# Kernel optimization log

Hardware: AMD Instinct MI355X
Metric: run time of the kernel (lower is better)

Reference implementation:

```python
import jax, jax.numpy as jnp
import numpy as np

B, S, U = 64, 64, 16
EMB = 10
D = U - 2 + 2 * EMB      # encoder d_model = 34
DD = 3                   # decoder d_model
FF = 4                   # dim_feedforward
NL = 4                   # num layers (enc and dec)
ENH = 2                  # encoder heads
WV, SV = 10000, 400      # word / syllable vocab sizes


def _ln(x, w, b, eps=1e-5):
    mu = jnp.mean(x, -1, keepdims=True)
    var = jnp.mean((x - mu) ** 2, -1, keepdims=True)
    return (x - mu) / jnp.sqrt(var + eps) * w + b


def _mha(xq, xkv, qkv_w, qkv_b, out_w, out_b, nhead, mask=None):
    d = xq.shape[-1]
    wq, wk, wv = jnp.split(qkv_w, 3, axis=0)
    bq, bk, bv = jnp.split(qkv_b, 3, axis=0)
    q = xq @ wq.T + bq
    k = xkv @ wk.T + bk
    v = xkv @ wv.T + bv
    b_, sq, sk = q.shape[0], q.shape[1], k.shape[1]
    dh = d // nhead
    q = q.reshape(b_, sq, nhead, dh)
    k = k.reshape(b_, sk, nhead, dh)
    v = v.reshape(b_, sk, nhead, dh)
    scores = jnp.einsum('bqhd,bkhd->bhqk', q, k) * (1.0 / np.sqrt(dh))
    if mask is not None:
        scores = scores + mask
    attn = jax.nn.softmax(scores, axis=-1)
    out = jnp.einsum('bhqk,bkhd->bqhd', attn, v).reshape(b_, sq, d)
    return out @ out_w.T + out_b


def _pos_encoding(batch, d_model):
    # Faithful to the original quirk: pe has shape [max_len, 1, d] and is added
    # to a batch-first [B,S,D] tensor as x + pe[:B]  ->  row b of pe is added
    # to ALL sequence positions of batch element b.
    pos = jnp.arange(batch, dtype=jnp.float32)[:, None]
    div = jnp.exp(jnp.arange(0, d_model, 2, dtype=jnp.float32) * (-np.log(10000.0) / d_model))
    ang = pos * div  # [B, D/2]
    pe = jnp.stack([jnp.sin(ang), jnp.cos(ang)], axis=-1).reshape(batch, d_model)
    return pe[:, None, :]  # [B,1,D]


def setup_inputs() -> dict:
    key = jax.random.key(0)
    ks = iter(jax.random.split(key, 64))

    def n(shape, s=0.1):
        return jax.random.normal(next(ks), shape, dtype=jnp.float32) * s

    base = jax.random.uniform(next(ks), (B, S, U), dtype=jnp.float32)
    widx = jax.random.randint(next(ks), (B, S), 0, WV).astype(jnp.float32)
    sidx = jax.random.randint(next(ks), (B, S), 0, SV).astype(jnp.float32)
    src = base.at[:, :, U - 2].set(widx).at[:, :, U - 1].set(sidx)
    return {
        'src': src,
        'word_emb': jax.random.uniform(next(ks), (WV, EMB), jnp.float32, -0.1, 0.1),
        'syll_emb': jax.random.uniform(next(ks), (SV, EMB), jnp.float32, -0.1, 0.1),
        'enc_qkv_w': n((NL, 3 * D, D)), 'enc_qkv_b': jnp.zeros((NL, 3 * D)),
        'enc_out_w': n((NL, D, D)), 'enc_out_b': jnp.zeros((NL, D)),
        'enc_ln1_w': jnp.ones((NL, D)), 'enc_ln1_b': jnp.zeros((NL, D)),
        'enc_lin1_w': n((NL, FF, D)), 'enc_lin1_b': jnp.zeros((NL, FF)),
        'enc_lin2_w': n((NL, D, FF)), 'enc_lin2_b': jnp.zeros((NL, D)),
        'enc_ln2_w': jnp.ones((NL, D)), 'enc_ln2_b': jnp.zeros((NL, D)),
        'norm_w': jnp.ones((D,)), 'norm_b': jnp.zeros((D,)),
        'eo_w': jax.random.uniform(next(ks), (DD, D), jnp.float32, -0.1, 0.1),
        'eo_b': jnp.zeros((DD,)),
        'dec_sa_qkv_w': n((NL, 3 * DD, DD)), 'dec_sa_qkv_b': jnp.zeros((NL, 3 * DD)),
        'dec_sa_out_w': n((NL, DD, DD)), 'dec_sa_out_b': jnp.zeros((NL, DD)),
        'dec_ln1_w': jnp.ones((NL, DD)), 'dec_ln1_b': jnp.zeros((NL, DD)),
        'dec_ca_qkv_w': n((NL, 3 * DD, DD)), 'dec_ca_qkv_b': jnp.zeros((NL, 3 * DD)),
        'dec_ca_out_w': n((NL, DD, DD)), 'dec_ca_out_b': jnp.zeros((NL, DD)),
        'dec_ln2_w': jnp.ones((NL, DD)), 'dec_ln2_b': jnp.zeros((NL, DD)),
        'dec_lin1_w': n((NL, FF, DD)), 'dec_lin1_b': jnp.zeros((NL, FF)),
        'dec_lin2_w': n((NL, DD, FF)), 'dec_lin2_b': jnp.zeros((NL, DD)),
        'dec_ln3_w': jnp.ones((NL, DD)), 'dec_ln3_b': jnp.zeros((NL, DD)),
    }


def reference(src, word_emb, syll_emb,
              enc_qkv_w, enc_qkv_b, enc_out_w, enc_out_b,
              enc_ln1_w, enc_ln1_b, enc_lin1_w, enc_lin1_b,
              enc_lin2_w, enc_lin2_b, enc_ln2_w, enc_ln2_b,
              norm_w, norm_b, eo_w, eo_b,
              dec_sa_qkv_w, dec_sa_qkv_b, dec_sa_out_w, dec_sa_out_b,
              dec_ln1_w, dec_ln1_b,
              dec_ca_qkv_w, dec_ca_qkv_b, dec_ca_out_w, dec_ca_out_b,
              dec_ln2_w, dec_ln2_b,
              dec_lin1_w, dec_lin1_b, dec_lin2_w, dec_lin2_b,
              dec_ln3_w, dec_ln3_b):
    b, s = src.shape[0], src.shape[1]
    # embed_lyrics
    widx = src[:, :, U - 2].astype(jnp.int32)
    sidx = src[:, :, U - 1].astype(jnp.int32)
    x = jnp.concatenate([src[:, :, :U - 2], word_emb[widx], syll_emb[sidx]], axis=2)  # [B,S,D]
    x = x + _pos_encoding(b, D)
    # TransformerEncoder (post-norm, relu, dropout=0) + final LayerNorm
    for l in range(NL):
        sa = _mha(x, x, enc_qkv_w[l], enc_qkv_b[l], enc_out_w[l], enc_out_b[l], ENH)
        x = _ln(x + sa, enc_ln1_w[l], enc_ln1_b[l])
        ff = jax.nn.relu(x @ enc_lin1_w[l].T + enc_lin1_b[l]) @ enc_lin2_w[l].T + enc_lin2_b[l]
        x = _ln(x + ff, enc_ln2_w[l], enc_ln2_b[l])
    x = _ln(x, norm_w, norm_b)
    memory = x @ eo_w.T + eo_b  # [B,S,3]

    causal = jnp.where(jnp.tril(jnp.ones((s, s), bool)), 0.0, -1e9).astype(jnp.float32)

    def decode(tgt):
        y = tgt
        for l in range(NL):
            sa = _mha(y, y, dec_sa_qkv_w[l], dec_sa_qkv_b[l], dec_sa_out_w[l], dec_sa_out_b[l], 1, causal)
            y = _ln(y + sa, dec_ln1_w[l], dec_ln1_b[l])
            ca = _mha(y, memory, dec_ca_qkv_w[l], dec_ca_qkv_b[l], dec_ca_out_w[l], dec_ca_out_b[l], 1)
            y = _ln(y + ca, dec_ln2_w[l], dec_ln2_b[l])
            ff = jax.nn.relu(y @ dec_lin1_w[l].T + dec_lin1_b[l]) @ dec_lin2_w[l].T + dec_lin2_b[l]
            y = _ln(y + ff, dec_ln3_w[l], dec_ln3_b[l])
        return y

    # mask, position i only depends on tgt[:, :i+1], so a fixed-size padded
    # buffer + scan computes identical values.
    def step(tgt, i):
        out_i = jax.lax.dynamic_slice_in_dim(decode(tgt), i, 1, axis=1)  # [B,1,3]
        return jax.lax.dynamic_update_slice(tgt, out_i, (0, i + 1, 0)), None

    tgt0 = jnp.zeros((b, s, DD), jnp.float32)
    tgt, _ = jax.lax.scan(step, tgt0, jnp.arange(s - 1))
    return jnp.concatenate([tgt, src[:, :, U - 2:U - 1], src[:, :, U - 1:U]], axis=2)
```

## Files before the change

### kernel.cpp

```cpp
#include <hip/hip_runtime.h>
#include <math.h>

#define B_ 64
#define S_ 64
#define U_ 16
#define EMB_ 10
#define D_ 34
#define DD_ 3
#define FF_ 4
#define NL_ 4

typedef float v2f __attribute__((ext_vector_type(2)));

__global__ __launch_bounds__(512) void enc_kernel(
    const float* __restrict__ src, const float* __restrict__ wemb,
    const float* __restrict__ semb,
    const float* __restrict__ qkv_w, const float* __restrict__ qkv_b,
    const float* __restrict__ out_w, const float* __restrict__ out_b,
    const float* __restrict__ ln1_w, const float* __restrict__ ln1_b,
    const float* __restrict__ lin1_w, const float* __restrict__ lin1_b,
    const float* __restrict__ lin2_w, const float* __restrict__ lin2_b,
    const float* __restrict__ ln2_w, const float* __restrict__ ln2_b,
    const float* __restrict__ norm_w, const float* __restrict__ norm_b,
    const float* __restrict__ eo_w, const float* __restrict__ eo_b,
    float* __restrict__ mem, float* __restrict__ out)
{
    const int b = blockIdx.x;
    const int tid = threadIdx.x;
    const int wv_ = tid >> 6;
    const int lane = tid & 63;

    __shared__ float xs[S_][D_ + 1];
    __shared__ float tmp[S_][D_ + 1];
    __shared__ float att[S_][D_ + 1];
    __shared__ __align__(16) float qsh[2][S_][21];
    __shared__ __align__(16) float ksh[2][S_][20];
    __shared__ __align__(16) float vsh[2][S_][20];
    __shared__ float ffh[S_][5];
    __shared__ float pacc[4][128][19];

    const float rs17 = 0.24253562503633297f;
    const float negln = -logf(10000.0f) / (float)D_;

    #pragma unroll
    for (int rr = 0; rr < 5; ++rr) {
        int idx = tid + rr * 512;
        if (idx < S_ * D_) {
            int pos = idx / D_, d = idx % D_;
            float v;
            if (d < U_ - 2) {
                v = src[(b * S_ + pos) * U_ + d];
            } else if (d < U_ - 2 + EMB_) {
                int wi = (int)src[(b * S_ + pos) * U_ + (U_ - 2)];
                v = wemb[wi * EMB_ + (d - (U_ - 2))];
            } else {
                int si = (int)src[(b * S_ + pos) * U_ + (U_ - 1)];
                v = semb[si * EMB_ + (d - (U_ - 2 + EMB_))];
            }
            int k = d >> 1;
            float div = __expf((float)(2 * k) * negln);
            float ang = (float)b * div;
            v += (d & 1) ? __cosf(ang) : __sinf(ang);
            xs[pos][d] = v;
        }
    }
    __syncthreads();

    for (int l = 0; l < NL_; ++l) {
        const float* Wq = qkv_w + l * 3 * D_ * D_;
        const float* Bq = qkv_b + l * 3 * D_;

        {
            v2f xr2[17];
            #pragma unroll
            for (int d2 = 0; d2 < 17; ++d2) {
                v2f t; t.x = xs[lane][2 * d2]; t.y = xs[lane][2 * d2 + 1];
                xr2[d2] = t;
            }
            #pragma unroll
            for (int rb = 0; rb < 13; ++rb) {
                int r = wv_ + (rb << 3);
                if (r < 3 * D_) {
                    int ru = __builtin_amdgcn_readfirstlane(r);
                    const v2f* w2 = (const v2f*)(Wq + ru * D_);
                    v2f a2; a2.x = Bq[ru]; a2.y = 0.f;
                    #pragma unroll
                    for (int d2 = 0; d2 < 17; ++d2)
                        a2 = __builtin_elementwise_fma(xr2[d2], w2[d2], a2);
                    float acc = a2.x + a2.y;
                    if (ru < D_)          { int h = (ru >= 17), dd = ru - h * 17; qsh[h][lane][dd] = acc; }
                    else if (ru < 2 * D_) { int rr2 = ru - D_;     int h = (rr2 >= 17), dd = rr2 - h * 17; ksh[h][lane][dd] = acc; }
                    else                  { int rr2 = ru - 2 * D_; int h = (rr2 >= 17), dd = rr2 - h * 17; vsh[h][lane][dd] = acc; }
                }
            }
        }
        __syncthreads();

        {
            int c = tid >> 7, hq = tid & 127;
            int h = hq >> 6, qi = hq & 63;
            float qv[17], acc[17];
            #pragma unroll
            for (int d = 0; d < 17; ++d) { qv[d] = qsh[h][qi][d]; acc[d] = 0.f; }
            float ssum = 0.f;
            int j0 = c * 16;
            #pragma unroll 4
            for (int jj = 0; jj < 16; ++jj) {
                int j = j0 + jj;
                const float4* kr = (const float4*)ksh[h][j];
                const float4* vr = (const float4*)vsh[h][j];
                float4 k0 = kr[0], k1 = kr[1], k2 = kr[2], k3 = kr[3];
                float  k16 = ksh[h][j][16];
                float4 v0 = vr[0], v1 = vr[1], v2 = vr[2], v3 = vr[3];
                float  v16 = vsh[h][j][16];
                float sE = qv[0]*k0.x + qv[2]*k0.z + qv[4]*k1.x + qv[6]*k1.z +
                           qv[8]*k2.x + qv[10]*k2.z + qv[12]*k3.x + qv[14]*k3.z;
                float sO = qv[1]*k0.y + qv[3]*k0.w + qv[5]*k1.y + qv[7]*k1.w +
                           qv[9]*k2.y + qv[11]*k2.w + qv[13]*k3.y + qv[15]*k3.w;
                float sc = sE + sO + qv[16]*k16;
                float e = __expf(sc * rs17);
                ssum += e;
                acc[0] += e*v0.x;  acc[1] += e*v0.y;  acc[2] += e*v0.z;  acc[3] += e*v0.w;
                acc[4] += e*v1.x;  acc[5] += e*v1.y;  acc[6] += e*v1.z;  acc[7] += e*v1.w;
                acc[8] += e*v2.x;  acc[9] += e*v2.y;  acc[10] += e*v2.z; acc[11] += e*v2.w;
                acc[12] += e*v3.x; acc[13] += e*v3.y; acc[14] += e*v3.z; acc[15] += e*v3.w;
                acc[16] += e*v16;
            }
            #pragma unroll
            for (int d = 0; d < 17; ++d) pacc[c][hq][d] = acc[d];
            pacc[c][hq][17] = ssum;
        }
        __syncthreads();

        if (tid < 128) {
            int h = tid >> 6, qi = tid & 63;
            int off = h * 17;
            float ssum = pacc[0][tid][17] + pacc[1][tid][17] +
                         pacc[2][tid][17] + pacc[3][tid][17];
            float inv = 1.f / ssum;
            #pragma unroll
            for (int d = 0; d < 17; ++d)
                att[qi][off + d] = (pacc[0][tid][d] + pacc[1][tid][d] +
                                    pacc[2][tid][d] + pacc[3][tid][d]) * inv;
        }
        __syncthreads();

        {
            v2f ar2[17];
            #pragma unroll
            for (int d2 = 0; d2 < 17; ++d2) {
                v2f t; t.x = att[lane][2 * d2]; t.y = att[lane][2 * d2 + 1];
                ar2[d2] = t;
            }
            const float* Wo = out_w + l * D_ * D_;
            const float* Bo = out_b + l * D_;
            #pragma unroll
            for (int rb = 0; rb < 5; ++rb) {
                int d = wv_ + (rb << 3);
                if (d < D_) {
                    int du = __builtin_amdgcn_readfirstlane(d);
                    const v2f* w2 = (const v2f*)(Wo + du * D_);
                    v2f a2; a2.x = Bo[du]; a2.y = 0.f;
                    #pragma unroll
                    for (int d2 = 0; d2 < 17; ++d2)
                        a2 = __builtin_elementwise_fma(ar2[d2], w2[d2], a2);
                    tmp[lane][du] = xs[lane][du] + a2.x + a2.y;
                }
            }
        }
        __syncthreads();

        {
            int row = tid >> 3, sub = tid & 7;
            float s = 0.f, sq = 0.f;
            #pragma unroll
            for (int d = sub; d < D_; d += 8) { float t = tmp[row][d]; s += t; sq = fmaf(t, t, sq); }
            #pragma unroll
            for (int m = 1; m < 8; m <<= 1) { s += __shfl_xor(s, m, 8); sq += __shfl_xor(sq, m, 8); }
            float mu = s * (1.0f / D_);
            float var = fmaf(sq, 1.0f / D_, -mu * mu);
            float rstd = rsqrtf(var + 1e-5f);
            #pragma unroll
            for (int d = sub; d < D_; d += 8)
                xs[row][d] = (tmp[row][d] - mu) * rstd * ln1_w[l * D_ + d] + ln1_b[l * D_ + d];
        }
        __syncthreads();

        if (wv_ < 4) {
            int fu = __builtin_amdgcn_readfirstlane(wv_);
            const v2f* w2 = (const v2f*)(lin1_w + l * FF_ * D_ + fu * D_);
            v2f a2; a2.x = lin1_b[l * FF_ + fu]; a2.y = 0.f;
            #pragma unroll
            for (int d2 = 0; d2 < 17; ++d2) {
                v2f t; t.x = xs[lane][2 * d2]; t.y = xs[lane][2 * d2 + 1];
                a2 = __builtin_elementwise_fma(t, w2[d2], a2);
            }
            ffh[lane][fu] = fmaxf(a2.x + a2.y, 0.f);
        }
        __syncthreads();

        {
            float h0 = ffh[lane][0], h1 = ffh[lane][1],
                  h2 = ffh[lane][2], h3 = ffh[lane][3];
            const float* W2 = lin2_w + l * D_ * FF_;
            const float* B2 = lin2_b + l * D_;
            #pragma unroll
            for (int rb = 0; rb < 5; ++rb) {
                int d = wv_ + (rb << 3);
                if (d < D_) {
                    int du = __builtin_amdgcn_readfirstlane(d);
                    const float* wrow = W2 + du * FF_;
                    float acc = fmaf(h0, wrow[0], fmaf(h1, wrow[1],
                                fmaf(h2, wrow[2], fmaf(h3, wrow[3], B2[du]))));
                    tmp[lane][du] = xs[lane][du] + acc;
                }
            }
        }
        __syncthreads();

        {
            int row = tid >> 3, sub = tid & 7;
            float s = 0.f, sq = 0.f;
            #pragma unroll
            for (int d = sub; d < D_; d += 8) { float t = tmp[row][d]; s += t; sq = fmaf(t, t, sq); }
            #pragma unroll
            for (int m = 1; m < 8; m <<= 1) { s += __shfl_xor(s, m, 8); sq += __shfl_xor(sq, m, 8); }
            float mu = s * (1.0f / D_);
            float var = fmaf(sq, 1.0f / D_, -mu * mu);
            float rstd = rsqrtf(var + 1e-5f);
            #pragma unroll
            for (int d = sub; d < D_; d += 8)
                xs[row][d] = (tmp[row][d] - mu) * rstd * ln2_w[l * D_ + d] + ln2_b[l * D_ + d];
        }
        __syncthreads();
    }

    {
        int row = tid >> 3, sub = tid & 7;
        float s = 0.f, sq = 0.f;
        #pragma unroll
        for (int d = sub; d < D_; d += 8) { float t = xs[row][d]; s += t; sq = fmaf(t, t, sq); }
        #pragma unroll
        for (int m = 1; m < 8; m <<= 1) { s += __shfl_xor(s, m, 8); sq += __shfl_xor(sq, m, 8); }
        float mu = s * (1.0f / D_);
        float var = fmaf(sq, 1.0f / D_, -mu * mu);
        float rstd = rsqrtf(var + 1e-5f);
        #pragma unroll
        for (int d = sub; d < D_; d += 8)
            tmp[row][d] = (xs[row][d] - mu) * rstd * norm_w[d] + norm_b[d];
    }
    __syncthreads();

    if (wv_ < 3) {
        int ru = __builtin_amdgcn_readfirstlane(wv_);
        const v2f* w2 = (const v2f*)(eo_w + ru * D_);
        v2f a2; a2.x = eo_b[ru]; a2.y = 0.f;
        #pragma unroll
        for (int d2 = 0; d2 < 17; ++d2) {
            v2f t; t.x = tmp[lane][2 * d2]; t.y = tmp[lane][2 * d2 + 1];
            a2 = __builtin_elementwise_fma(t, w2[d2], a2);
        }
        mem[(b * S_ + lane) * DD_ + ru] = a2.x + a2.y;
    }

    if (tid < S_) {
        out[(b * S_ + tid) * 5 + 3] = src[(b * S_ + tid) * U_ + (U_ - 2)];
        out[(b * S_ + tid) * 5 + 4] = src[(b * S_ + tid) * U_ + (U_ - 1)];
    }
}

#define PIN(x) asm volatile("" : "+v"(x))

template <int N> struct IC { static constexpr int value = N; };

template <int CTRL>
__device__ __forceinline__ void dpp4(float& a, float& b, float& c, float& d) {
    int ta = __builtin_amdgcn_update_dpp(0, __float_as_int(a), CTRL, 0xf, 0xf, true);
    int tb = __builtin_amdgcn_update_dpp(0, __float_as_int(b), CTRL, 0xf, 0xf, true);
    int tc = __builtin_amdgcn_update_dpp(0, __float_as_int(c), CTRL, 0xf, 0xf, true);
    int td = __builtin_amdgcn_update_dpp(0, __float_as_int(d), CTRL, 0xf, 0xf, true);
    a += __int_as_float(ta);
    b += __int_as_float(tb);
    c += __int_as_float(tc);
    d += __int_as_float(td);
}

__device__ __forceinline__ void red16_4(float& a, float& b, float& c, float& d) {
    dpp4<0x111>(a, b, c, d);
    dpp4<0x112>(a, b, c, d);
    dpp4<0x114>(a, b, c, d);
    dpp4<0x118>(a, b, c, d);
}

template <int L>
__device__ __forceinline__ float rlane(float v) {
    return __int_as_float(__builtin_amdgcn_readlane(__float_as_int(v), L));
}

__device__ __forceinline__ void ln3e(float z0, float z1, float z2,
                                     float w0, float w1, float w2,
                                     float b0, float b1, float b2,
                                     float& o0, float& o1, float& o2) {
    float s1 = (z0 + z1) + z2;
    float s2 = fmaf(z0, z0, fmaf(z1, z1, z2 * z2));
    float mu = s1 * (1.0f / 3.0f);
    float vpe = fmaf(s2, (1.0f / 3.0f), fmaf(-mu, mu, 1e-5f));
    float rstd = __builtin_amdgcn_rsqf(vpe);
    o0 = fmaf(z0 - mu, rstd * w0, b0);
    o1 = fmaf(z1 - mu, rstd * w1, b1);
    o2 = fmaf(z2 - mu, rstd * w2, b2);
}

__global__ __launch_bounds__(64, 1) void dec_kernel(
    const float* __restrict__ mem,
    const float* __restrict__ sa_qkv_w, const float* __restrict__ sa_qkv_b,
    const float* __restrict__ sa_out_w, const float* __restrict__ sa_out_b,
    const float* __restrict__ gln1_w, const float* __restrict__ gln1_b,
    const float* __restrict__ ca_qkv_w, const float* __restrict__ ca_qkv_b,
    const float* __restrict__ ca_out_w, const float* __restrict__ ca_out_b,
    const float* __restrict__ gln2_w, const float* __restrict__ gln2_b,
    const float* __restrict__ l1_w, const float* __restrict__ l1_b,
    const float* __restrict__ l2_w, const float* __restrict__ l2_b,
    const float* __restrict__ gln3_w, const float* __restrict__ gln3_b,
    float* __restrict__ out)
{
    const int b = blockIdx.x;
    const int lane = threadIdx.x;
    const float LOG2E = 1.4426950408889634f;
    const float rs3 = 0.5773502691896258f;
    const float QS = rs3 * LOG2E;

    float Wsq[NL_][6][3], Bsq[NL_][6];
    float Wvp[NL_][3][3], Bvp[NL_][3];
    float Bso[NL_][3];
    float N1w[NL_][3], N1bF[NL_][3];
    float N2w[NL_][3], N2bF[NL_][3];
    float wcu[NL_][3];
    float swcu[NL_];
    float cbb[NL_];
    float cvp[NL_][3];
    float W1N[NL_][4][3], b1n[NL_][4];
    float W2r[NL_][3][4];
    float N3w[NL_][3], N3b[NL_][3];

    #pragma unroll
    for (int l = 0; l < NL_; ++l) {
        #pragma unroll
        for (int r = 0; r < 6; ++r) {
            float sc = (r < 3) ? QS : 1.0f;
            Bsq[l][r] = sa_qkv_b[l * 9 + r] * sc;
            #pragma unroll
            for (int c = 0; c < 3; ++c) Wsq[l][r][c] = sa_qkv_w[l * 27 + r * 3 + c] * sc;
        }
        #pragma unroll
        for (int r = 0; r < 3; ++r) {
            float w0 = sa_out_w[l * 9 + r * 3 + 0];
            float w1 = sa_out_w[l * 9 + r * 3 + 1];
            float w2 = sa_out_w[l * 9 + r * 3 + 2];
            Bvp[l][r] = w0 * sa_qkv_b[l * 9 + 6] + w1 * sa_qkv_b[l * 9 + 7] + w2 * sa_qkv_b[l * 9 + 8];
            #pragma unroll
            for (int c = 0; c < 3; ++c)
                Wvp[l][r][c] = w0 * sa_qkv_w[l * 27 + 6 * 3 + c] +
                               w1 * sa_qkv_w[l * 27 + 7 * 3 + c] +
                               w2 * sa_qkv_w[l * 27 + 8 * 3 + c];
        }
        #pragma unroll
        for (int r = 0; r < 3; ++r) {
            Bso[l][r]  = sa_out_b[l * 3 + r];
            N1w[l][r]  = gln1_w[l * 3 + r];
            N1bF[l][r] = gln1_b[l * 3 + r] + ca_out_b[l * 3 + r];
            N2w[l][r]  = gln2_w[l * 3 + r];
            N2bF[l][r] = gln2_b[l * 3 + r] + l2_b[l * 3 + r];
            N3w[l][r]  = gln3_w[l * 3 + r];
            N3b[l][r]  = gln3_b[l * 3 + r];
        }
        #pragma unroll
        for (int j = 0; j < 4; ++j) {
            #pragma unroll
            for (int c = 0; c < 3; ++c)
                W1N[l][j][c] = l1_w[l * 12 + j * 3 + c] * gln2_w[l * 3 + c];
            b1n[l][j] = l1_w[l * 12 + j * 3 + 0] * gln2_b[l * 3 + 0] +
                        l1_w[l * 12 + j * 3 + 1] * gln2_b[l * 3 + 1] +
                        l1_w[l * 12 + j * 3 + 2] * gln2_b[l * 3 + 2] + l1_b[l * 4 + j];
        }
        #pragma unroll
        for (int r = 0; r < 3; ++r)
            #pragma unroll
            for (int j = 0; j < 4; ++j)
                W2r[l][r][j] = l2_w[l * 12 + r * 4 + j];
    }

    float m0 = mem[(b * S_ + lane) * DD_ + 0];
    float m1 = mem[(b * S_ + lane) * DD_ + 1];
    float m2 = mem[(b * S_ + lane) * DD_ + 2];

    #pragma unroll
    for (int l = 0; l < NL_; ++l) {
        float ck[3], cv[3], cuv[3];
        #pragma unroll
        for (int r = 0; r < 3; ++r) {
            ck[r] = ca_qkv_w[l * 27 + (3 + r) * 3 + 0] * m0 +
                    ca_qkv_w[l * 27 + (3 + r) * 3 + 1] * m1 +
                    ca_qkv_w[l * 27 + (3 + r) * 3 + 2] * m2 + ca_qkv_b[l * 9 + 3 + r];
            cv[r] = ca_qkv_w[l * 27 + (6 + r) * 3 + 0] * m0 +
                    ca_qkv_w[l * 27 + (6 + r) * 3 + 1] * m1 +
                    ca_qkv_w[l * 27 + (6 + r) * 3 + 2] * m2 + ca_qkv_b[l * 9 + 6 + r];
        }
        #pragma unroll
        for (int s = 0; s < 3; ++s)
            cuv[s] = QS * (ca_qkv_w[l * 27 + 0 + s] * ck[0] +
                           ca_qkv_w[l * 27 + 3 + s] * ck[1] +
                           ca_qkv_w[l * 27 + 6 + s] * ck[2]);
        float cbv = QS * (ca_qkv_b[l * 9 + 0] * ck[0] +
                          ca_qkv_b[l * 9 + 1] * ck[1] +
                          ca_qkv_b[l * 9 + 2] * ck[2]);
        #pragma unroll
        for (int r = 0; r < 3; ++r)
            cvp[l][r] = ca_out_w[l * 9 + r * 3 + 0] * cv[0] +
                        ca_out_w[l * 9 + r * 3 + 1] * cv[1] +
                        ca_out_w[l * 9 + r * 3 + 2] * cv[2];
        #pragma unroll
        for (int r = 0; r < 3; ++r) wcu[l][r] = cuv[r] * N1w[l][r];
        swcu[l] = wcu[l][0] + wcu[l][1] + wcu[l][2];
        cbb[l]  = cbv + cuv[0] * gln1_b[l * 3 + 0] + cuv[1] * gln1_b[l * 3 + 1]
                      + cuv[2] * gln1_b[l * 3 + 2];
    }

    #pragma unroll
    for (int l = 0; l < NL_; ++l) {
        #pragma unroll
        for (int r = 0; r < 6; ++r) {
            PIN(Bsq[l][r]);
            #pragma unroll
            for (int c = 0; c < 3; ++c) PIN(Wsq[l][r][c]);
        }
        PIN(swcu[l]); PIN(cbb[l]);
        #pragma unroll
        for (int r = 0; r < 3; ++r) {
            PIN(Bvp[l][r]); PIN(Bso[l][r]);
            PIN(N1w[l][r]); PIN(N1bF[l][r]); PIN(N2w[l][r]); PIN(N2bF[l][r]);
            PIN(N3w[l][r]); PIN(N3b[l][r]);
            PIN(wcu[l][r]); PIN(cvp[l][r]);
            #pragma unroll
            for (int c = 0; c < 3; ++c) PIN(Wvp[l][r][c]);
            #pragma unroll
            for (int j = 0; j < 4; ++j) PIN(W2r[l][r][j]);
        }
        #pragma unroll
        for (int j = 0; j < 4; ++j) {
            PIN(b1n[l][j]);
            #pragma unroll
            for (int c = 0; c < 3; ++c) PIN(W1N[l][j][c]);
        }
    }

    float sk[NL_][3] = {{0.f}}, sv[NL_][3] = {{0.f}};

    if (lane < 3) out[(b * S_ + 0) * 5 + lane] = 0.f;

    float y0 = 0.f, y1 = 0.f, y2 = 0.f;

    auto run_range = [&](int ibeg, int iend, auto nstc) {
        constexpr int NST = decltype(nstc)::value;
        constexpr int RL = (NST == 4) ? 15 : (NST == 5) ? 31 : 63;
        for (int i = ibeg; i < iend; ++i) {
            float msa = (lane <= i) ? 0.f : -1.0e30f;
            bool isme = (lane == i);
            #pragma unroll
            for (int l = 0; l < NL_; ++l) {
                float q[3], kn[3], vp[3];
                #pragma unroll
                for (int r = 0; r < 3; ++r) {
                    kn[r] = fmaf(Wsq[l][3 + r][0], y0, fmaf(Wsq[l][3 + r][1], y1, fmaf(Wsq[l][3 + r][2], y2, Bsq[l][3 + r])));
                    q[r]  = fmaf(Wsq[l][r][0], y0, fmaf(Wsq[l][r][1], y1, fmaf(Wsq[l][r][2], y2, Bsq[l][r])));
                    vp[r] = fmaf(Wvp[l][r][0], y0, fmaf(Wvp[l][r][1], y1, fmaf(Wvp[l][r][2], y2, Bvp[l][r])));
                }
                if (isme) {
                    #pragma unroll
                    for (int r = 0; r < 3; ++r) { sk[l][r] = kn[r]; sv[l][r] = vp[r]; }
                }
                float sc = fmaf(q[0], sk[l][0], fmaf(q[1], sk[l][1], fmaf(q[2], sk[l][2], msa)));
                float e = __builtin_amdgcn_exp2f(sc);
                float se = e;
                float sa0 = e * sv[l][0];
                float sa1 = e * sv[l][1];
                float sa2 = e * sv[l][2];
                red16_4(se, sa0, sa1, sa2);
                if constexpr (NST >= 5) dpp4<0x142>(se, sa0, sa1, sa2);
                if constexpr (NST >= 6) dpp4<0x143>(se, sa0, sa1, sa2);
                float es = rlane<RL>(se);
                float S0 = rlane<RL>(sa0), S1 = rlane<RL>(sa1), S2 = rlane<RL>(sa2);
                float yb0 = y0 + Bso[l][0], yb1 = y1 + Bso[l][1], yb2 = y2 + Bso[l][2];
                float z0 = fmaf(yb0, es, S0), z1 = fmaf(yb1, es, S1), z2v = fmaf(yb2, es, S2);
                float ee = es * es;

                float s1m = (z0 + z1) + z2v;
                float mu = s1m * (1.0f / 3.0f);
                float zw = fmaf(z0, wcu[l][0], fmaf(z1, wcu[l][1], z2v * wcu[l][2]));
                float inner = fmaf(-mu, swcu[l], zw);
                float s2m = fmaf(z0, z0, fmaf(z1, z1, z2v * z2v));
                float vpe = fmaf(s2m, (1.0f / 3.0f), fmaf(-mu, mu, 1e-5f * ee));
                float rstd1 = __builtin_amdgcn_rsqf(vpe);
                float sc2 = fmaf(rstd1, inner, cbb[l]);
                float e2 = __builtin_amdgcn_exp2f(sc2);
                float ce = e2;
                float ca0 = e2 * cvp[l][0];
                float ca1 = e2 * cvp[l][1];
                float ca2 = e2 * cvp[l][2];
                red16_4(ce, ca0, ca1, ca2);
                dpp4<0x142>(ce, ca0, ca1, ca2);
                dpp4<0x143>(ce, ca0, ca1, ca2);
                float yc0 = fmaf(z0 - mu, rstd1 * N1w[l][0], N1bF[l][0]);
                float yc1 = fmaf(z1 - mu, rstd1 * N1w[l][1], N1bF[l][1]);
                float yc2 = fmaf(z2v - mu, rstd1 * N1w[l][2], N1bF[l][2]);
                float cs = rlane<63>(ce);
                float C0 = rlane<63>(ca0), C1 = rlane<63>(ca1), C2 = rlane<63>(ca2);
                float g0 = fmaf(yc0, cs, C0), g1 = fmaf(yc1, cs, C1), g2 = fmaf(yc2, cs, C2);
                float cee = cs * cs;

                float t1m = (g0 + g1) + g2;
                float mu2 = t1m * (1.0f / 3.0f);
                float c20 = g0 - mu2, c21 = g1 - mu2, c22 = g2 - mu2;
                float t2m = fmaf(g0, g0, fmaf(g1, g1, g2 * g2));
                float vpe2 = fmaf(t2m, (1.0f / 3.0f), fmaf(-mu2, mu2, 1e-5f * cee));
                float rstd2 = __builtin_amdgcn_rsqf(vpe2);
                float d0 = fmaf(W1N[l][0][0], c20, fmaf(W1N[l][0][1], c21, W1N[l][0][2] * c22));
                float d1 = fmaf(W1N[l][1][0], c20, fmaf(W1N[l][1][1], c21, W1N[l][1][2] * c22));
                float d2 = fmaf(W1N[l][2][0], c20, fmaf(W1N[l][2][1], c21, W1N[l][2][2] * c22));
                float d3 = fmaf(W1N[l][3][0], c20, fmaf(W1N[l][3][1], c21, W1N[l][3][2] * c22));
                float h0 = fmaxf(fmaf(rstd2, d0, b1n[l][0]), 0.f);
                float h1 = fmaxf(fmaf(rstd2, d1, b1n[l][1]), 0.f);
                float h2 = fmaxf(fmaf(rstd2, d2, b1n[l][2]), 0.f);
                float h3 = fmaxf(fmaf(rstd2, d3, b1n[l][3]), 0.f);
                float yf0 = fmaf(c20, rstd2 * N2w[l][0], N2bF[l][0]);
                float yf1 = fmaf(c21, rstd2 * N2w[l][1], N2bF[l][1]);
                float yf2 = fmaf(c22, rstd2 * N2w[l][2], N2bF[l][2]);
                float f0 = fmaf(W2r[l][0][0], h0, fmaf(W2r[l][0][1], h1, fmaf(W2r[l][0][2], h2, fmaf(W2r[l][0][3], h3, yf0))));
                float f1 = fmaf(W2r[l][1][0], h0, fmaf(W2r[l][1][1], h1, fmaf(W2r[l][1][2], h2, fmaf(W2r[l][1][3], h3, yf1))));
                float f2 = fmaf(W2r[l][2][0], h0, fmaf(W2r[l][2][1], h1, fmaf(W2r[l][2][2], h2, fmaf(W2r[l][2][3], h3, yf2))));
                ln3e(f0, f1, f2,
                     N3w[l][0], N3w[l][1], N3w[l][2], N3b[l][0], N3b[l][1], N3b[l][2],
                     y0, y1, y2);
            }
            if (lane == 0) {
                out[(b * S_ + i + 1) * 5 + 0] = y0;
                out[(b * S_ + i + 1) * 5 + 1] = y1;
                out[(b * S_ + i + 1) * 5 + 2] = y2;
            }
        }
    };

    run_range(0, 15, IC<4>{});
    run_range(15, 31, IC<5>{});
    run_range(31, S_ - 1, IC<6>{});
}

extern "C" void kernel_launch(void* const* d_in, const int* in_sizes, int n_in,
                              void* d_out, int out_size, void* d_ws, size_t ws_size,
                              hipStream_t stream) {
    const float* src  = (const float*)d_in[0];
    const float* wemb = (const float*)d_in[1];
    const float* semb = (const float*)d_in[2];

    float* mem = (float*)d_ws;
    float* out = (float*)d_out;

    enc_kernel<<<B_, 512, 0, stream>>>(
        src, wemb, semb,
        (const float*)d_in[3],  (const float*)d_in[4],
        (const float*)d_in[5],  (const float*)d_in[6],
        (const float*)d_in[7],  (const float*)d_in[8],
        (const float*)d_in[9],  (const float*)d_in[10],
        (const float*)d_in[11], (const float*)d_in[12],
        (const float*)d_in[13], (const float*)d_in[14],
        (const float*)d_in[15], (const float*)d_in[16],
        (const float*)d_in[17], (const float*)d_in[18],
        mem, out);

    dec_kernel<<<B_, 64, 0, stream>>>(
        mem,
        (const float*)d_in[19], (const float*)d_in[20],
        (const float*)d_in[21], (const float*)d_in[22],
        (const float*)d_in[23], (const float*)d_in[24],
        (const float*)d_in[25], (const float*)d_in[26],
        (const float*)d_in[27], (const float*)d_in[28],
        (const float*)d_in[29], (const float*)d_in[30],
        (const float*)d_in[31], (const float*)d_in[32],
        (const float*)d_in[33], (const float*)d_in[34],
        (const float*)d_in[35], (const float*)d_in[36],
        out);
}
```

Measured before the change: 310.1 us.

## Fuse encoder and decoder into one launch with global flag handoff

Merges the encoder and decoder kernels into a single 128-block launch. Blocks 0-63 run the encoder and signal completion through a global atomic counter, while blocks 64-127 load decoder weights and then spin until all encoder blocks are done. This is meant to remove the second kernel launch and inter-kernel gap, and to overlap decoder weight setup with encoder work. In exchange, the decoder blocks must wait for all 64 encoder blocks rather than only their own batch element. The decoder now runs with 512-thread blocks of which 448 threads exit immediately, and progress depends on all 128 blocks being resident at once.

New measurement: 693.2 us. +123.5%, slower.

```diff
diff --git a/kernel.cpp b/kernel.cpp
--- a/kernel.cpp
+++ b/kernel.cpp
@@ -11,263 +11,6 @@
 #define NL_ 4
 
 typedef float v2f __attribute__((ext_vector_type(2)));
-
-__global__ __launch_bounds__(512) void enc_kernel(
-    const float* __restrict__ src, const float* __restrict__ wemb,
-    const float* __restrict__ semb,
-    const float* __restrict__ qkv_w, const float* __restrict__ qkv_b,
-    const float* __restrict__ out_w, const float* __restrict__ out_b,
-    const float* __restrict__ ln1_w, const float* __restrict__ ln1_b,
-    const float* __restrict__ lin1_w, const float* __restrict__ lin1_b,
-    const float* __restrict__ lin2_w, const float* __restrict__ lin2_b,
-    const float* __restrict__ ln2_w, const float* __restrict__ ln2_b,
-    const float* __restrict__ norm_w, const float* __restrict__ norm_b,
-    const float* __restrict__ eo_w, const float* __restrict__ eo_b,
-    float* __restrict__ mem, float* __restrict__ out)
-{
-    const int b = blockIdx.x;
-    const int tid = threadIdx.x;
-    const int wv_ = tid >> 6;
-    const int lane = tid & 63;
-
-    __shared__ float xs[S_][D_ + 1];
-    __shared__ float tmp[S_][D_ + 1];
-    __shared__ float att[S_][D_ + 1];
-    __shared__ __align__(16) float qsh[2][S_][21];
-    __shared__ __align__(16) float ksh[2][S_][20];
-    __shared__ __align__(16) float vsh[2][S_][20];
-    __shared__ float ffh[S_][5];
-    __shared__ float pacc[4][128][19];
-
-    const float rs17 = 0.24253562503633297f;
-    const float negln = -logf(10000.0f) / (float)D_;
-
-    #pragma unroll
-    for (int rr = 0; rr < 5; ++rr) {
-        int idx = tid + rr * 512;
-        if (idx < S_ * D_) {
-            int pos = idx / D_, d = idx % D_;
-            float v;
-            if (d < U_ - 2) {
-                v = src[(b * S_ + pos) * U_ + d];
-            } else if (d < U_ - 2 + EMB_) {
-                int wi = (int)src[(b * S_ + pos) * U_ + (U_ - 2)];
-                v = wemb[wi * EMB_ + (d - (U_ - 2))];
-            } else {
-                int si = (int)src[(b * S_ + pos) * U_ + (U_ - 1)];
-                v = semb[si * EMB_ + (d - (U_ - 2 + EMB_))];
-            }
-            int k = d >> 1;
-            float div = __expf((float)(2 * k) * negln);
-            float ang = (float)b * div;
-            v += (d & 1) ? __cosf(ang) : __sinf(ang);
-            xs[pos][d] = v;
-        }
-    }
-    __syncthreads();
-
-    for (int l = 0; l < NL_; ++l) {
-        const float* Wq = qkv_w + l * 3 * D_ * D_;
-        const float* Bq = qkv_b + l * 3 * D_;
-
-        {
-            v2f xr2[17];
-            #pragma unroll
-            for (int d2 = 0; d2 < 17; ++d2) {
-                v2f t; t.x = xs[lane][2 * d2]; t.y = xs[lane][2 * d2 + 1];
-                xr2[d2] = t;
-            }
-            #pragma unroll
-            for (int rb = 0; rb < 13; ++rb) {
-                int r = wv_ + (rb << 3);
-                if (r < 3 * D_) {
-                    int ru = __builtin_amdgcn_readfirstlane(r);
-                    const v2f* w2 = (const v2f*)(Wq + ru * D_);
-                    v2f a2; a2.x = Bq[ru]; a2.y = 0.f;
-                    #pragma unroll
-                    for (int d2 = 0; d2 < 17; ++d2)
-                        a2 = __builtin_elementwise_fma(xr2[d2], w2[d2], a2);
-                    float acc = a2.x + a2.y;
-                    if (ru < D_)          { int h = (ru >= 17), dd = ru - h * 17; qsh[h][lane][dd] = acc; }
-                    else if (ru < 2 * D_) { int rr2 = ru - D_;     int h = (rr2 >= 17), dd = rr2 - h * 17; ksh[h][lane][dd] = acc; }
-                    else                  { int rr2 = ru - 2 * D_; int h = (rr2 >= 17), dd = rr2 - h * 17; vsh[h][lane][dd] = acc; }
-                }
-            }
-        }
-        __syncthreads();
-
-        {
-            int c = tid >> 7, hq = tid & 127;
-            int h = hq >> 6, qi = hq & 63;
-            float qv[17], acc[17];
-            #pragma unroll
-            for (int d = 0; d < 17; ++d) { qv[d] = qsh[h][qi][d]; acc[d] = 0.f; }
-            float ssum = 0.f;
-            int j0 = c * 16;
-            #pragma unroll 4
-            for (int jj = 0; jj < 16; ++jj) {
-                int j = j0 + jj;
-                const float4* kr = (const float4*)ksh[h][j];
-                const float4* vr = (const float4*)vsh[h][j];
-                float4 k0 = kr[0], k1 = kr[1], k2 = kr[2], k3 = kr[3];
-                float  k16 = ksh[h][j][16];
-                float4 v0 = vr[0], v1 = vr[1], v2 = vr[2], v3 = vr[3];
-                float  v16 = vsh[h][j][16];
-                float sE = qv[0]*k0.x + qv[2]*k0.z + qv[4]*k1.x + qv[6]*k1.z +
-                           qv[8]*k2.x + qv[10]*k2.z + qv[12]*k3.x + qv[14]*k3.z;
-                float sO = qv[1]*k0.y + qv[3]*k0.w + qv[5]*k1.y + qv[7]*k1.w +
-                           qv[9]*k2.y + qv[11]*k2.w + qv[13]*k3.y + qv[15]*k3.w;
-                float sc = sE + sO + qv[16]*k16;
-                float e = __expf(sc * rs17);
-                ssum += e;
-                acc[0] += e*v0.x;  acc[1] += e*v0.y;  acc[2] += e*v0.z;  acc[3] += e*v0.w;
-                acc[4] += e*v1.x;  acc[5] += e*v1.y;  acc[6] += e*v1.z;  acc[7] += e*v1.w;
-                acc[8] += e*v2.x;  acc[9] += e*v2.y;  acc[10] += e*v2.z; acc[11] += e*v2.w;
-                acc[12] += e*v3.x; acc[13] += e*v3.y; acc[14] += e*v3.z; acc[15] += e*v3.w;
-                acc[16] += e*v16;
-            }
-            #pragma unroll
-            for (int d = 0; d < 17; ++d) pacc[c][hq][d] = acc[d];
-            pacc[c][hq][17] = ssum;
-        }
-        __syncthreads();
-
-        if (tid < 128) {
-            int h = tid >> 6, qi = tid & 63;
-            int off = h * 17;
-            float ssum = pacc[0][tid][17] + pacc[1][tid][17] +
-                         pacc[2][tid][17] + pacc[3][tid][17];
-            float inv = 1.f / ssum;
-            #pragma unroll
-            for (int d = 0; d < 17; ++d)
-                att[qi][off + d] = (pacc[0][tid][d] + pacc[1][tid][d] +
-                                    pacc[2][tid][d] + pacc[3][tid][d]) * inv;
-        }
-        __syncthreads();
-
-        {
-            v2f ar2[17];
-            #pragma unroll
-            for (int d2 = 0; d2 < 17; ++d2) {
-                v2f t; t.x = att[lane][2 * d2]; t.y = att[lane][2 * d2 + 1];
-                ar2[d2] = t;
-            }
-            const float* Wo = out_w + l * D_ * D_;
-            const float* Bo = out_b + l * D_;
-            #pragma unroll
-            for (int rb = 0; rb < 5; ++rb) {
-                int d = wv_ + (rb << 3);
-                if (d < D_) {
-                    int du = __builtin_amdgcn_readfirstlane(d);
-                    const v2f* w2 = (const v2f*)(Wo + du * D_);
-                    v2f a2; a2.x = Bo[du]; a2.y = 0.f;
-                    #pragma unroll
-                    for (int d2 = 0; d2 < 17; ++d2)
-                        a2 = __builtin_elementwise_fma(ar2[d2], w2[d2], a2);
-                    tmp[lane][du] = xs[lane][du] + a2.x + a2.y;
-                }
-            }
-        }
-        __syncthreads();
-
-        {
-            int row = tid >> 3, sub = tid & 7;
-            float s = 0.f, sq = 0.f;
-            #pragma unroll
-            for (int d = sub; d < D_; d += 8) { float t = tmp[row][d]; s += t; sq = fmaf(t, t, sq); }
-            #pragma unroll
-            for (int m = 1; m < 8; m <<= 1) { s += __shfl_xor(s, m, 8); sq += __shfl_xor(sq, m, 8); }
-            float mu = s * (1.0f / D_);
-            float var = fmaf(sq, 1.0f / D_, -mu * mu);
-            float rstd = rsqrtf(var + 1e-5f);
-            #pragma unroll
-            for (int d = sub; d < D_; d += 8)
-                xs[row][d] = (tmp[row][d] - mu) * rstd * ln1_w[l * D_ + d] + ln1_b[l * D_ + d];
-        }
-        __syncthreads();
-
-        if (wv_ < 4) {
-            int fu = __builtin_amdgcn_readfirstlane(wv_);
-            const v2f* w2 = (const v2f*)(lin1_w + l * FF_ * D_ + fu * D_);
-            v2f a2; a2.x = lin1_b[l * FF_ + fu]; a2.y = 0.f;
-            #pragma unroll
-            for (int d2 = 0; d2 < 17; ++d2) {
-                v2f t; t.x = xs[lane][2 * d2]; t.y = xs[lane][2 * d2 + 1];
-                a2 = __builtin_elementwise_fma(t, w2[d2], a2);
-            }
-            ffh[lane][fu] = fmaxf(a2.x + a2.y, 0.f);
-        }
-        __syncthreads();
-
-        {
-            float h0 = ffh[lane][0], h1 = ffh[lane][1],
-                  h2 = ffh[lane][2], h3 = ffh[lane][3];
-            const float* W2 = lin2_w + l * D_ * FF_;
-            const float* B2 = lin2_b + l * D_;
-            #pragma unroll
-            for (int rb = 0; rb < 5; ++rb) {
-                int d = wv_ + (rb << 3);
-                if (d < D_) {
-                    int du = __builtin_amdgcn_readfirstlane(d);
-                    const float* wrow = W2 + du * FF_;
-                    float acc = fmaf(h0, wrow[0], fmaf(h1, wrow[1],
-                                fmaf(h2, wrow[2], fmaf(h3, wrow[3], B2[du]))));
-                    tmp[lane][du] = xs[lane][du] + acc;
-                }
-            }
-        }
-        __syncthreads();
-
-        {
-            int row = tid >> 3, sub = tid & 7;
-            float s = 0.f, sq = 0.f;
-            #pragma unroll
-            for (int d = sub; d < D_; d += 8) { float t = tmp[row][d]; s += t; sq = fmaf(t, t, sq); }
-            #pragma unroll
-            for (int m = 1; m < 8; m <<= 1) { s += __shfl_xor(s, m, 8); sq += __shfl_xor(sq, m, 8); }
-            float mu = s * (1.0f / D_);
-            float var = fmaf(sq, 1.0f / D_, -mu * mu);
-            float rstd = rsqrtf(var + 1e-5f);
-            #pragma unroll
-            for (int d = sub; d < D_; d += 8)
-                xs[row][d] = (tmp[row][d] - mu) * rstd * ln2_w[l * D_ + d] + ln2_b[l * D_ + d];
-        }
-        __syncthreads();
-    }
-
-    {
-        int row = tid >> 3, sub = tid & 7;
-        float s = 0.f, sq = 0.f;
-        #pragma unroll
-        for (int d = sub; d < D_; d += 8) { float t = xs[row][d]; s += t; sq = fmaf(t, t, sq); }
-        #pragma unroll
-        for (int m = 1; m < 8; m <<= 1) { s += __shfl_xor(s, m, 8); sq += __shfl_xor(sq, m, 8); }
-        float mu = s * (1.0f / D_);
-        float var = fmaf(sq, 1.0f / D_, -mu * mu);
-        float rstd = rsqrtf(var + 1e-5f);
-        #pragma unroll
-        for (int d = sub; d < D_; d += 8)
-            tmp[row][d] = (xs[row][d] - mu) * rstd * norm_w[d] + norm_b[d];
-    }
-    __syncthreads();
-
-    if (wv_ < 3) {
-        int ru = __builtin_amdgcn_readfirstlane(wv_);
-        const v2f* w2 = (const v2f*)(eo_w + ru * D_);
-        v2f a2; a2.x = eo_b[ru]; a2.y = 0.f;
-        #pragma unroll
-        for (int d2 = 0; d2 < 17; ++d2) {
-            v2f t; t.x = tmp[lane][2 * d2]; t.y = tmp[lane][2 * d2 + 1];
-            a2 = __builtin_elementwise_fma(t, w2[d2], a2);
-        }
-        mem[(b * S_ + lane) * DD_ + ru] = a2.x + a2.y;
-    }
-
-    if (tid < S_) {
-        out[(b * S_ + tid) * 5 + 3] = src[(b * S_ + tid) * U_ + (U_ - 2)];
-        out[(b * S_ + tid) * 5 + 4] = src[(b * S_ + tid) * U_ + (U_ - 1)];
-    }
-}
 
 #define PIN(x) asm volatile("" : "+v"(x))
 
@@ -311,8 +54,20 @@
     o2 = fmaf(z2 - mu, rstd * w2, b2);
 }
 
-__global__ __launch_bounds__(64, 1) void dec_kernel(
-    const float* __restrict__ mem,
+__device__ int g_flagA;
+__device__ int g_flagB;
+
+__global__ __launch_bounds__(512) void fused_kernel(
+    const float* __restrict__ src, const float* __restrict__ wemb,
+    const float* __restrict__ semb,
+    const float* __restrict__ qkv_w, const float* __restrict__ qkv_b,
+    const float* __restrict__ out_w, const float* __restrict__ out_b,
+    const float* __restrict__ ln1_w, const float* __restrict__ ln1_b,
+    const float* __restrict__ lin1_w, const float* __restrict__ lin1_b,
+    const float* __restrict__ lin2_w, const float* __restrict__ lin2_b,
+    const float* __restrict__ ln2_w, const float* __restrict__ ln2_b,
+    const float* __restrict__ norm_w, const float* __restrict__ norm_b,
+    const float* __restrict__ eo_w, const float* __restrict__ eo_b,
     const float* __restrict__ sa_qkv_w, const float* __restrict__ sa_qkv_b,
     const float* __restrict__ sa_out_w, const float* __restrict__ sa_out_b,
     const float* __restrict__ gln1_w, const float* __restrict__ gln1_b,
@@ -322,10 +77,264 @@
     const float* __restrict__ l1_w, const float* __restrict__ l1_b,
     const float* __restrict__ l2_w, const float* __restrict__ l2_b,
     const float* __restrict__ gln3_w, const float* __restrict__ gln3_b,
-    float* __restrict__ out)
+    float* __restrict__ mem, float* __restrict__ out)
 {
-    const int b = blockIdx.x;
-    const int lane = threadIdx.x;
+    const int tid = threadIdx.x;
+
+    if (blockIdx.x < 64) {
+        const int b = blockIdx.x;
+        const int wv_ = tid >> 6;
+        const int lane = tid & 63;
+
+        __shared__ float xs[S_][D_ + 1];
+        __shared__ float tmp[S_][D_ + 1];
+        __shared__ float att[S_][D_ + 1];
+        __shared__ __align__(16) float qsh[2][S_][21];
+        __shared__ __align__(16) float ksh[2][S_][20];
+        __shared__ __align__(16) float vsh[2][S_][20];
+        __shared__ float ffh[S_][5];
+        __shared__ float pacc[4][128][19];
+
+        const float rs17 = 0.24253562503633297f;
+        const float negln = -logf(10000.0f) / (float)D_;
+
+        #pragma unroll
+        for (int rr = 0; rr < 5; ++rr) {
+            int idx = tid + rr * 512;
+            if (idx < S_ * D_) {
+                int pos = idx / D_, d = idx % D_;
+                float v;
+                if (d < U_ - 2) {
+                    v = src[(b * S_ + pos) * U_ + d];
+                } else if (d < U_ - 2 + EMB_) {
+                    int wi = (int)src[(b * S_ + pos) * U_ + (U_ - 2)];
+                    v = wemb[wi * EMB_ + (d - (U_ - 2))];
+                } else {
+                    int si = (int)src[(b * S_ + pos) * U_ + (U_ - 1)];
+                    v = semb[si * EMB_ + (d - (U_ - 2 + EMB_))];
+                }
+                int k = d >> 1;
+                float div = __expf((float)(2 * k) * negln);
+                float ang = (float)b * div;
+                v += (d & 1) ? __cosf(ang) : __sinf(ang);
+                xs[pos][d] = v;
+            }
+        }
+        __syncthreads();
+
+        for (int l = 0; l < NL_; ++l) {
+            const float* Wq = qkv_w + l * 3 * D_ * D_;
+            const float* Bq = qkv_b + l * 3 * D_;
+
+            {
+                v2f xr2[17];
+                #pragma unroll
+                for (int d2 = 0; d2 < 17; ++d2) {
+                    v2f t; t.x = xs[lane][2 * d2]; t.y = xs[lane][2 * d2 + 1];
+                    xr2[d2] = t;
+                }
+                #pragma unroll
+                for (int rb = 0; rb < 13; ++rb) {
+                    int r = wv_ + (rb << 3);
+                    if (r < 3 * D_) {
+                        int ru = __builtin_amdgcn_readfirstlane(r);
+                        const v2f* w2 = (const v2f*)(Wq + ru * D_);
+                        v2f a2; a2.x = Bq[ru]; a2.y = 0.f;
+                        #pragma unroll
+                        for (int d2 = 0; d2 < 17; ++d2)
+                            a2 = __builtin_elementwise_fma(xr2[d2], w2[d2], a2);
+                        float acc = a2.x + a2.y;
+                        if (ru < D_)          { int h = (ru >= 17), dd = ru - h * 17; qsh[h][lane][dd] = acc; }
+                        else if (ru < 2 * D_) { int rr2 = ru - D_;     int h = (rr2 >= 17), dd = rr2 - h * 17; ksh[h][lane][dd] = acc; }
+                        else                  { int rr2 = ru - 2 * D_; int h = (rr2 >= 17), dd = rr2 - h * 17; vsh[h][lane][dd] = acc; }
+                    }
+                }
+            }
+            __syncthreads();
+
+            {
+                int c = tid >> 7, hq = tid & 127;
+                int h = hq >> 6, qi = hq & 63;
+                float qv[17], acc[17];
+                #pragma unroll
+                for (int d = 0; d < 17; ++d) { qv[d] = qsh[h][qi][d]; acc[d] = 0.f; }
+                float ssum = 0.f;
+                int j0 = c * 16;
+                #pragma unroll 4
+                for (int jj = 0; jj < 16; ++jj) {
+                    int j = j0 + jj;
+                    const float4* kr = (const float4*)ksh[h][j];
+                    const float4* vr = (const float4*)vsh[h][j];
+                    float4 k0 = kr[0], k1 = kr[1], k2 = kr[2], k3 = kr[3];
+                    float  k16 = ksh[h][j][16];
+                    float4 v0 = vr[0], v1 = vr[1], v2 = vr[2], v3 = vr[3];
+                    float  v16 = vsh[h][j][16];
+                    float sE = qv[0]*k0.x + qv[2]*k0.z + qv[4]*k1.x + qv[6]*k1.z +
+                               qv[8]*k2.x + qv[10]*k2.z + qv[12]*k3.x + qv[14]*k3.z;
+                    float sO = qv[1]*k0.y + qv[3]*k0.w + qv[5]*k1.y + qv[7]*k1.w +
+                               qv[9]*k2.y + qv[11]*k2.w + qv[13]*k3.y + qv[15]*k3.w;
+                    float sc = sE + sO + qv[16]*k16;
+                    float e = __expf(sc * rs17);
+                    ssum += e;
+                    acc[0] += e*v0.x;  acc[1] += e*v0.y;  acc[2] += e*v0.z;  acc[3] += e*v0.w;
+                    acc[4] += e*v1.x;  acc[5] += e*v1.y;  acc[6] += e*v1.z;  acc[7] += e*v1.w;
+                    acc[8] += e*v2.x;  acc[9] += e*v2.y;  acc[10] += e*v2.z; acc[11] += e*v2.w;
+                    acc[12] += e*v3.x; acc[13] += e*v3.y; acc[14] += e*v3.z; acc[15] += e*v3.w;
+                    acc[16] += e*v16;
+                }
+                #pragma unroll
+                for (int d = 0; d < 17; ++d) pacc[c][hq][d] = acc[d];
+                pacc[c][hq][17] = ssum;
+            }
+            __syncthreads();
+
+            if (tid < 128) {
+                int h = tid >> 6, qi = tid & 63;
+                int off = h * 17;
+                float ssum = pacc[0][tid][17] + pacc[1][tid][17] +
+                             pacc[2][tid][17] + pacc[3][tid][17];
+                float inv = 1.f / ssum;
+                #pragma unroll
+                for (int d = 0; d < 17; ++d)
+                    att[qi][off + d] = (pacc[0][tid][d] + pacc[1][tid][d] +
+                                        pacc[2][tid][d] + pacc[3][tid][d]) * inv;
+            }
+            __syncthreads();
+
+            {
+                v2f ar2[17];
+                #pragma unroll
+                for (int d2 = 0; d2 < 17; ++d2) {
+                    v2f t; t.x = att[lane][2 * d2]; t.y = att[lane][2 * d2 + 1];
+                    ar2[d2] = t;
+                }
+                const float* Wo = out_w + l * D_ * D_;
+                const float* Bo = out_b + l * D_;
+                #pragma unroll
+                for (int rb = 0; rb < 5; ++rb) {
+                    int d = wv_ + (rb << 3);
+                    if (d < D_) {
+                        int du = __builtin_amdgcn_readfirstlane(d);
+                        const v2f* w2 = (const v2f*)(Wo + du * D_);
+                        v2f a2; a2.x = Bo[du]; a2.y = 0.f;
+                        #pragma unroll
+                        for (int d2 = 0; d2 < 17; ++d2)
+                            a2 = __builtin_elementwise_fma(ar2[d2], w2[d2], a2);
+                        tmp[lane][du] = xs[lane][du] + a2.x + a2.y;
+                    }
+                }
+            }
+            __syncthreads();
+
+            {
+                int row = tid >> 3, sub = tid & 7;
+                float s = 0.f, sq = 0.f;
+                #pragma unroll
+                for (int d = sub; d < D_; d += 8) { float t = tmp[row][d]; s += t; sq = fmaf(t, t, sq); }
+                #pragma unroll
+                for (int m = 1; m < 8; m <<= 1) { s += __shfl_xor(s, m, 8); sq += __shfl_xor(sq, m, 8); }
+                float mu = s * (1.0f / D_);
+                float var = fmaf(sq, 1.0f / D_, -mu * mu);
+                float rstd = rsqrtf(var + 1e-5f);
+                #pragma unroll
+                for (int d = sub; d < D_; d += 8)
+                    xs[row][d] = (tmp[row][d] - mu) * rstd * ln1_w[l * D_ + d] + ln1_b[l * D_ + d];
+            }
+            __syncthreads();
+
+            if (wv_ < 4) {
+                int fu = __builtin_amdgcn_readfirstlane(wv_);
+                const v2f* w2 = (const v2f*)(lin1_w + l * FF_ * D_ + fu * D_);
+                v2f a2; a2.x = lin1_b[l * FF_ + fu]; a2.y = 0.f;
+                #pragma unroll
+                for (int d2 = 0; d2 < 17; ++d2) {
+                    v2f t; t.x = xs[lane][2 * d2]; t.y = xs[lane][2 * d2 + 1];
+                    a2 = __builtin_elementwise_fma(t, w2[d2], a2);
+                }
+                ffh[lane][fu] = fmaxf(a2.x + a2.y, 0.f);
+            }
+            __syncthreads();
+
+            {
+                float h0 = ffh[lane][0], h1 = ffh[lane][1],
+                      h2 = ffh[lane][2], h3 = ffh[lane][3];
+                const float* W2 = lin2_w + l * D_ * FF_;
+                const float* B2 = lin2_b + l * D_;
+                #pragma unroll
+                for (int rb = 0; rb < 5; ++rb) {
+                    int d = wv_ + (rb << 3);
+                    if (d < D_) {
+                        int du = __builtin_amdgcn_readfirstlane(d);
+                        const float* wrow = W2 + du * FF_;
+                        float acc = fmaf(h0, wrow[0], fmaf(h1, wrow[1],
+                                    fmaf(h2, wrow[2], fmaf(h3, wrow[3], B2[du]))));
+                        tmp[lane][du] = xs[lane][du] + acc;
+                    }
+                }
+            }
+            __syncthreads();
+
+            {
+                int row = tid >> 3, sub = tid & 7;
+                float s = 0.f, sq = 0.f;
+                #pragma unroll
+                for (int d = sub; d < D_; d += 8) { float t = tmp[row][d]; s += t; sq = fmaf(t, t, sq); }
+                #pragma unroll
+                for (int m = 1; m < 8; m <<= 1) { s += __shfl_xor(s, m, 8); sq += __shfl_xor(sq, m, 8); }
+                float mu = s * (1.0f / D_);
+                float var = fmaf(sq, 1.0f / D_, -mu * mu);
+                float rstd = rsqrtf(var + 1e-5f);
+                #pragma unroll
+                for (int d = sub; d < D_; d += 8)
+                    xs[row][d] = (tmp[row][d] - mu) * rstd * ln2_w[l * D_ + d] + ln2_b[l * D_ + d];
+            }
+            __syncthreads();
+        }
+
+        {
+            int row = tid >> 3, sub = tid & 7;
+            float s = 0.f, sq = 0.f;
+            #pragma unroll
+            for (int d = sub; d < D_; d += 8) { float t = xs[row][d]; s += t; sq = fmaf(t, t, sq); }
+            #pragma unroll
+            for (int m = 1; m < 8; m <<= 1) { s += __shfl_xor(s, m, 8); sq += __shfl_xor(sq, m, 8); }
+            float mu = s * (1.0f / D_);
+            float var = fmaf(sq, 1.0f / D_, -mu * mu);
+            float rstd = rsqrtf(var + 1e-5f);
+            #pragma unroll
+            for (int d = sub; d < D_; d += 8)
+                tmp[row][d] = (xs[row][d] - mu) * rstd * norm_w[d] + norm_b[d];
+        }
+        __syncthreads();
+
+        if (wv_ < 3) {
+            int ru = __builtin_amdgcn_readfirstlane(wv_);
+            const v2f* w2 = (const v2f*)(eo_w + ru * D_);
+            v2f a2; a2.x = eo_b[ru]; a2.y = 0.f;
+            #pragma unroll
+            for (int d2 = 0; d2 < 17; ++d2) {
+                v2f t; t.x = tmp[lane][2 * d2]; t.y = tmp[lane][2 * d2 + 1];
+                a2 = __builtin_elementwise_fma(t, w2[d2], a2);
+            }
+            mem[(b * S_ + lane) * DD_ + ru] = a2.x + a2.y;
+        }
+
+        if (tid < S_) {
+            out[(b * S_ + tid) * 5 + 3] = src[(b * S_ + tid) * U_ + (U_ - 2)];
+            out[(b * S_ + tid) * 5 + 4] = src[(b * S_ + tid) * U_ + (U_ - 1)];
+        }
+
+        __syncthreads();
+        if (tid == 0) {
+            __threadfence();
+            __hip_atomic_fetch_add(&g_flagA, 1, __ATOMIC_RELEASE, __HIP_MEMORY_SCOPE_AGENT);
+        }
+        return;
+    }
+
+    if (tid >= 64) return;
+    const int b = blockIdx.x - 64;
+    const int lane = tid;
     const float LOG2E = 1.4426950408889634f;
     const float rs3 = 0.5773502691896258f;
     const float QS = rs3 * LOG2E;
@@ -389,6 +398,11 @@
             for (int j = 0; j < 4; ++j)
                 W2r[l][r][j] = l2_w[l * 12 + r * 4 + j];
     }
+
+    while (__hip_atomic_load(&g_flagA, __ATOMIC_ACQUIRE, __HIP_MEMORY_SCOPE_AGENT) < 64) {
+        __builtin_amdgcn_s_sleep(8);
+    }
+    asm volatile("" ::: "memory");
 
     float m0 = mem[(b * S_ + lane) * DD_ + 0];
     float m1 = mem[(b * S_ + lane) * DD_ + 1];
@@ -553,6 +567,14 @@
     run_range(0, 15, IC<4>{});
     run_range(15, 31, IC<5>{});
     run_range(31, S_ - 1, IC<6>{});
+
+    if (lane == 0) {
+        int old = __hip_atomic_fetch_add(&g_flagB, 1, __ATOMIC_ACQ_REL, __HIP_MEMORY_SCOPE_AGENT);
+        if (old == 63) {
+            __hip_atomic_store(&g_flagA, 0, __ATOMIC_RELAXED, __HIP_MEMORY_SCOPE_AGENT);
+            __hip_atomic_store(&g_flagB, 0, __ATOMIC_RELAXED, __HIP_MEMORY_SCOPE_AGENT);
+        }
+    }
 }
 
 extern "C" void kernel_launch(void* const* d_in, const int* in_sizes, int n_in,
@@ -565,7 +587,7 @@
     float* mem = (float*)d_ws;
     float* out = (float*)d_out;
 
-    enc_kernel<<<B_, 512, 0, stream>>>(
+    fused_kernel<<<128, 512, 0, stream>>>(
         src, wemb, semb,
         (const float*)d_in[3],  (const float*)d_in[4],
         (const float*)d_in[5],  (const float*)d_in[6],
@@ -575,10 +597,6 @@
         (const float*)d_in[13], (const float*)d_in[14],
         (const float*)d_in[15], (const float*)d_in[16],
         (const float*)d_in[17], (const float*)d_in[18],
-        mem, out);
-
-    dec_kernel<<<B_, 64, 0, stream>>>(
-        mem,
         (const float*)d_in[19], (const float*)d_in[20],
         (const float*)d_in[21], (const float*)d_in[22],
         (const float*)d_in[23], (const float*)d_in[24],
@@ -588,5 +606,5 @@
         (const float*)d_in[31], (const float*)d_in[32],
         (const float*)d_in[33], (const float*)d_in[34],
         (const float*)d_in[35], (const float*)d_in[36],
-        out);
+        mem, out);
 }
```
